# Performance work log

Hardware: AMD Instinct MI355X
Metric: run time of the kernel (lower is better)

## Reference

```python
import jax, jax.numpy as jnp
import numpy as np

N = 50000          # neuron_count
NNZ = 1_600_000    # edges (avg degree 32)
B = 32             # batch
L = 3              # CONNECTOME_LAYER_NUMBER


def setup_inputs() -> dict:
    key = jax.random.key(0)
    k1, k2, k3, k4, k5 = jax.random.split(key, 5)
    x = jax.random.normal(k1, (B, N), dtype=jnp.float32)
    adj_vals = jax.random.uniform(k2, (NNZ,), dtype=jnp.float32)
    w_vals = jax.random.uniform(k3, (NNZ,), dtype=jnp.float32)
    bias = jnp.ones((N,), dtype=jnp.float32)
    row = jax.random.randint(k4, (NNZ,), 0, N, dtype=jnp.int32)
    col = jax.random.randint(k5, (NNZ,), 0, N, dtype=jnp.int32)
    return {"x": x, "adj_vals": adj_vals, "w_vals": w_vals, "bias": bias,
            "row": row, "col": col}


def _spmm(vals, row, col, dense, n):
    # (sparse NxN) @ dense [N, B] via gather + segment_sum scatter
    contrib = vals[:, None] * dense[col]          # [nnz, B]
    return jax.ops.segment_sum(contrib, row, num_segments=n)


def reference(x, adj_vals, w_vals, bias, row, col):
    # Original per layer: x = ((A @ W) @ x^T)^T + bias.
    # We use associativity: (A @ W) @ x^T == A @ (W @ x^T), avoiding the
    # explicit SpGEMM while computing the same linear map.
    n = bias.shape[0]
    xt = x.T                                      # [N, B]
    for _ in range(L):
        wx = _spmm(w_vals, row, col, xt, n)       # W @ x^T -> [N, B]
        xt = _spmm(adj_vals, row, col, wx, n)     # A @ (W @ x^T)
        xt = xt + bias[:, None]                   # broadcast bias over batch
    return xt.T                                   # [B, N]
```

## Files before the change

kernel.cpp:

```cpp
#include <hip/hip_runtime.h>


#define NN 50000
#define NNZ_E 1600000
#define NB (NN * 32)
#define CHUNK 3072
#define NBLK1 ((NNZ_E + CHUNK - 1) / CHUNK)
#define NBIN ((NN + 127) / 128)
#define CAP2 5120
#define BCAP1 6144
#define LENE (NBIN * BCAP1)
#define BCAP 6144
#define LENP (NBIN * BCAP)
#define TIN_BLKS 196

__device__ __forceinline__ int clampi(int v, int hi) {
    v = v < 0 ? 0 : v;
    return v > hi ? hi : v;
}

__device__ __forceinline__ unsigned short f2h(float v) {
    union { _Float16 h; unsigned short u; } cv;
    cv.h = (_Float16)v;
    return cv.u;
}

__device__ __forceinline__ float kv_val(unsigned kv) {
    union { unsigned short u; _Float16 h; } cv;
    cv.u = (unsigned short)(kv >> 16);
    return (float)cv.h;
}

__global__ __launch_bounds__(256) void pass1_kernel(
        const int* __restrict__ row, const int* __restrict__ col,
        const float* __restrict__ a, const float* __restrict__ w,
        int* __restrict__ cursor, uint2* __restrict__ e1,
        const float* __restrict__ x, _Float16* __restrict__ xt) {
    __shared__ int h[NBIN];
    __shared__ int hscan[NBIN];
    __shared__ int hoff[NBIN];
    __shared__ int wsum[4];
    __shared__ unsigned sBuf[2 * CHUNK];
    int blk = blockIdx.x, tid = threadIdx.x;

    if (blk >= NBLK1) {
        _Float16* tl = (_Float16*)sBuf;
        int n0 = (blk - NBLK1) * 256;
        int n = n0 + tid;
#pragma unroll 8
        for (int b = 0; b < 32; ++b) {
            float v = (n < NN) ? x[b * NN + n] : 0.0f;
            tl[tid * 33 + b] = (_Float16)v;
        }
        __syncthreads();
#pragma unroll
        for (int k = 0; k < 4; ++k) {
            int o = (tid + 256 * k) * 8;
            int nl = o >> 5;
            int b0 = o & 31;
            int nn = n0 + nl;
            if (nn < NN) {
                union { uint4 u4; _Float16 hh[8]; } pk;
#pragma unroll
                for (int j = 0; j < 8; ++j) pk.hh[j] = tl[nl * 33 + b0 + j];
                *(uint4*)&xt[nn * 32 + b0] = pk.u4;
            }
        }
        return;
    }

    int base = blk * CHUNK;
    int n = NNZ_E - base; if (n > CHUNK) n = CHUNK;
    int nv = n >> 2;
    unsigned* sKey = sBuf;
    unsigned* sAW  = sBuf + CHUNK;

    for (int j = tid; j < NBIN; j += 256) h[j] = 0;
    __syncthreads();

    int rr[12], cc[12];
    unsigned aw2[12];
    int ne = 0;
    const int4*   rv4 = (const int4*)row;
    const int4*   cv4 = (const int4*)col;
    const float4* av4 = (const float4*)a;
    const float4* wv4 = (const float4*)w;
    int b4 = base >> 2;
    for (int t4 = tid; t4 < nv; t4 += 256) {
        int4 r = rv4[b4 + t4];
        int4 c = cv4[b4 + t4];
        float4 af = av4[b4 + t4];
        float4 wf = wv4[b4 + t4];
        rr[ne] = r.x; cc[ne] = c.x; aw2[ne] = ((unsigned)f2h(af.x) << 16) | f2h(wf.x); ++ne;
        rr[ne] = r.y; cc[ne] = c.y; aw2[ne] = ((unsigned)f2h(af.y) << 16) | f2h(wf.y); ++ne;
        rr[ne] = r.z; cc[ne] = c.z; aw2[ne] = ((unsigned)f2h(af.z) << 16) | f2h(wf.z); ++ne;
        rr[ne] = r.w; cc[ne] = c.w; aw2[ne] = ((unsigned)f2h(af.w) << 16) | f2h(wf.w); ++ne;
    }
    for (int i = 0; i < ne; ++i)
        atomicAdd(&h[clampi(rr[i], NN - 1) >> 7], 1);
    __syncthreads();

    int j0 = tid * 2, j1 = tid * 2 + 1;
    int c0 = (j0 < NBIN) ? h[j0] : 0;
    int c1 = (j1 < NBIN) ? h[j1] : 0;
    int tsum = c0 + c1;
    int lane = tid & 63, wid = tid >> 6;
    int inc = tsum;
#pragma unroll
    for (int off = 1; off < 64; off <<= 1) {
        int u = __shfl_up(inc, off, 64);
        if (lane >= off) inc += u;
    }
    if (lane == 63) wsum[wid] = inc;
    __syncthreads();
    int wo = 0;
#pragma unroll
    for (int q = 0; q < 4; ++q) if (q < wid) wo += wsum[q];
    int ex = wo + inc - tsum;

    if (j0 < NBIN) {
        hscan[j0] = ex;
        h[j0] = ex;
        int b0 = c0 ? atomicAdd(&cursor[j0], c0) : 0;
        hoff[j0] = j0 * BCAP1 + clampi(b0, BCAP1 - 1);
    }
    if (j1 < NBIN) {
        hscan[j1] = ex + c0;
        h[j1] = ex + c0;
        int b1 = c1 ? atomicAdd(&cursor[j1], c1) : 0;
        hoff[j1] = j1 * BCAP1 + clampi(b1, BCAP1 - 1);
    }
    __syncthreads();
    for (int i = 0; i < ne; ++i) {
        int r = clampi(rr[i], NN - 1);
        int c = clampi(cc[i], NN - 1);
        int bin = r >> 7;
        int p = atomicAdd(&h[bin], 1);
        p = clampi(p, n - 1);
        sKey[p] = ((unsigned)r << 16) | (unsigned)c;
        sAW[p] = aw2[i];
    }
    __syncthreads();
    for (int p = tid; p < n; p += 256) {
        unsigned key = sKey[p];
        int bin = (int)(key >> 23);
        int d = clampi(hoff[bin] + (p - hscan[bin]), LENE - 1);
        e1[d] = make_uint2(key, sAW[p]);
    }
}

__global__ __launch_bounds__(256) void pass2_kernel(
        const uint2* __restrict__ e1, const int* __restrict__ cursor,
        unsigned* __restrict__ kvA2, unsigned* __restrict__ kvW2,
        unsigned* __restrict__ row_desc) {
    __shared__ int rh[128];
    __shared__ int rs[128];
    __shared__ int cur[128];
    int bin = blockIdx.x, tid = threadIdx.x;
    int r0 = bin << 7;
    int rows = NN - r0; if (rows > 128) rows = 128;
    int ebase = bin * BCAP1;
    int size = clampi(cursor[bin], CAP2);
    int pbase = bin * BCAP;

    if (tid < 128) rh[tid] = 0;
    __syncthreads();
    for (int i = tid; i < size; i += 256)
        atomicAdd(&rh[(e1[ebase + i].x >> 16) & 127], 1);
    __syncthreads();
    int cnt  = (tid < 128) ? rh[tid] : 0;
    int plen = (cnt + 7) & ~7;
    if (tid < 128) rs[tid] = plen;
    __syncthreads();
    for (int off = 1; off < 128; off <<= 1) {
        int t = (tid >= off && tid < 128) ? rs[tid - off] : 0;
        __syncthreads();
        if (tid < 128) rs[tid] += t;
        __syncthreads();
    }
    int rofs = (tid < 128) ? clampi(rs[tid] - plen, BCAP - 8) : 0;
    if (tid < 128) cur[tid] = rofs;
    if (tid < rows)
        row_desc[r0 + tid] = (unsigned)(pbase + rofs) | ((unsigned)(plen >> 3) << 24);
    __syncthreads();
    for (int i = tid; i < size; i += 256) {
        uint2 e = e1[ebase + i];
        unsigned key = e.x;
        unsigned aw  = e.y;
        int rl = (key >> 16) & 127;
        int p = atomicAdd(&cur[rl], 1);
        p = clampi(p, BCAP - 1);
        unsigned c = key & 0xFFFFu;
        kvA2[pbase + p] = (aw & 0xFFFF0000u) | c;
        kvW2[pbase + p] = (aw << 16) | c;
    }
    __syncthreads();
    if (tid < rows) {
        int pl = (rh[tid] + 7) & ~7;
        for (int q = rh[tid]; q < pl; ++q) {
            int d = clampi(rofs + q, BCAP - 1);
            kvA2[pbase + d] = 0u;
            kvW2[pbase + d] = 0u;
        }
    }
}

template <int WITH_BIAS, int FINAL>
__global__ __launch_bounds__(256) void spmm_kernel(
        const uint2* __restrict__ kv2, const unsigned* __restrict__ row_desc,
        const unsigned* __restrict__ in32, unsigned* __restrict__ out32,
        const float* __restrict__ bias, float outScale, float biasScale,
        float* __restrict__ outf) {
    int t = blockIdx.x * 256 + threadIdx.x;
    int r = t >> 4;
    int l = t & 15;
    if (r >= NN) return;
    unsigned d = row_desc[r];
    int niter = (int)(d >> 24);
    int base2 = clampi((int)(d & 0xFFFFFFu), LENP - 8) >> 1;
    float accL = 0.0f, accH = 0.0f;
    uint2 k2[4];
    if (niter > 0) {
#pragma unroll
        for (int q = 0; q < 4; ++q) k2[q] = kv2[base2 + q];
    }
    for (int it = 0; it < niter; ++it) {
        unsigned k[8];
#pragma unroll
        for (int q = 0; q < 4; ++q) { k[2 * q] = k2[q].x; k[2 * q + 1] = k2[q].y; }
        unsigned gd[8];
#pragma unroll
        for (int j = 0; j < 8; ++j) gd[j] = in32[((k[j] & 0xFFFFu) << 4) + l];
        if (it + 1 < niter) {
            int nb2 = base2 + (it + 1) * 4;
#pragma unroll
            for (int q = 0; q < 4; ++q) k2[q] = kv2[nb2 + q];
        }
#pragma unroll
        for (int j = 0; j < 8; ++j) {
            float v = kv_val(k[j]);
            union { unsigned u; _Float16 h[2]; } cv;
            cv.u = gd[j];
            accL += v * (float)cv.h[0];
            accH += v * (float)cv.h[1];
        }
    }
    float rL = accL * outScale, rH = accH * outScale;
    if (WITH_BIAS) {
        float bb = bias[r] * biasScale;
        rL += bb; rH += bb;
    }
    if (FINAL) {
        outf[(2 * l) * NN + r]     = rL * 16777216.0f;
        outf[(2 * l + 1) * NN + r] = rH * 16777216.0f;
    } else {
        union { unsigned u; _Float16 h[2]; } o;
        o.h[0] = (_Float16)rL;
        o.h[1] = (_Float16)rH;
        out32[(r << 4) + l] = o.u;
    }
}

extern "C" void kernel_launch(void* const* d_in, const int* in_sizes, int n_in,
                              void* d_out, int out_size, void* d_ws, size_t ws_size,
                              hipStream_t stream) {
    const float* x        = (const float*)d_in[0];
    const float* adj_vals = (const float*)d_in[1];
    const float* w_vals   = (const float*)d_in[2];
    const float* bias     = (const float*)d_in[3];
    const int*   row      = (const int*)d_in[4];
    const int*   col      = (const int*)d_in[5];
    float* out = (float*)d_out;

    uint2*     e1        = (uint2*)d_ws;
    unsigned*  kvA2      = (unsigned*)(e1 + LENE);
    unsigned*  kvW2      = kvA2 + LENP;
    _Float16*  xt16      = (_Float16*)(kvW2 + LENP);
    _Float16*  tmp16     = xt16 + NB;
    int*       cursor    = (int*)(tmp16 + NB);
    unsigned*  row_desc  = (unsigned*)(cursor + NBIN + 8);

    const int BS = 256;
    const int grid_spmm = (NN * 16 + BS - 1) / BS;

    hipMemsetAsync(cursor, 0, NBIN * sizeof(int), stream);
    pass1_kernel<<<NBLK1 + TIN_BLKS, BS, 0, stream>>>(row, col, adj_vals, w_vals,
                                                      cursor, e1, x, xt16);
    pass2_kernel<<<NBIN, BS, 0, stream>>>(e1, cursor, kvA2, kvW2, row_desc);

    const uint2* kvA = (const uint2*)kvA2;
    const uint2* kvW = (const uint2*)kvW2;
    const unsigned* xt32  = (const unsigned*)xt16;
    unsigned*       xt32w = (unsigned*)xt16;
    const unsigned* tm32  = (const unsigned*)tmp16;
    unsigned*       tm32w = (unsigned*)tmp16;

    const float r256 = 1.0f / 256.0f;
    spmm_kernel<0, 0><<<grid_spmm, BS, 0, stream>>>(kvW, row_desc, xt32, tm32w,
                                                    nullptr, 1.0f, 0.0f, nullptr);
    spmm_kernel<1, 0><<<grid_spmm, BS, 0, stream>>>(kvA, row_desc, tm32, xt32w,
                                                    bias, r256, 1.0f / 256.0f, nullptr);
    spmm_kernel<0, 0><<<grid_spmm, BS, 0, stream>>>(kvW, row_desc, xt32, tm32w,
                                                    nullptr, 1.0f, 0.0f, nullptr);
    spmm_kernel<1, 0><<<grid_spmm, BS, 0, stream>>>(kvA, row_desc, tm32, xt32w,
                                                    bias, r256, 1.0f / 65536.0f, nullptr);
    spmm_kernel<0, 0><<<grid_spmm, BS, 0, stream>>>(kvW, row_desc, xt32, tm32w,
                                                    nullptr, 1.0f, 0.0f, nullptr);
    spmm_kernel<1, 1><<<grid_spmm, BS, 0, stream>>>(kvA, row_desc, tm32, xt32w,
                                                    bias, r256, 1.0f / 16777216.0f, out);
}
```

Baseline: 231.6 us.

## Scatter edges directly to global bins, dropping shared-memory staging and scan

Result: slower. 238.0 us (+2.7%).

```diff
diff --git a/kernel.cpp b/kernel.cpp
--- a/kernel.cpp
+++ b/kernel.cpp
@@ -36,11 +36,7 @@
         const float* __restrict__ a, const float* __restrict__ w,
         int* __restrict__ cursor, uint2* __restrict__ e1,
         const float* __restrict__ x, _Float16* __restrict__ xt) {
-    __shared__ int h[NBIN];
-    __shared__ int hscan[NBIN];
-    __shared__ int hoff[NBIN];
-    __shared__ int wsum[4];
-    __shared__ unsigned sBuf[2 * CHUNK];
+    __shared__ unsigned sBuf[256 * 33 / 2 + 8];
     int blk = blockIdx.x, tid = threadIdx.x;
 
     if (blk >= NBLK1) {
@@ -69,11 +65,10 @@
         return;
     }
 
+    int* h = (int*)sBuf;
     int base = blk * CHUNK;
     int n = NNZ_E - base; if (n > CHUNK) n = CHUNK;
     int nv = n >> 2;
-    unsigned* sKey = sBuf;
-    unsigned* sAW  = sBuf + CHUNK;
 
     for (int j = tid; j < NBIN; j += 256) h[j] = 0;
     __syncthreads();
@@ -101,51 +96,25 @@
     __syncthreads();
 
     int j0 = tid * 2, j1 = tid * 2 + 1;
-    int c0 = (j0 < NBIN) ? h[j0] : 0;
-    int c1 = (j1 < NBIN) ? h[j1] : 0;
-    int tsum = c0 + c1;
-    int lane = tid & 63, wid = tid >> 6;
-    int inc = tsum;
-#pragma unroll
-    for (int off = 1; off < 64; off <<= 1) {
-        int u = __shfl_up(inc, off, 64);
-        if (lane >= off) inc += u;
-    }
-    if (lane == 63) wsum[wid] = inc;
-    __syncthreads();
-    int wo = 0;
-#pragma unroll
-    for (int q = 0; q < 4; ++q) if (q < wid) wo += wsum[q];
-    int ex = wo + inc - tsum;
-
     if (j0 < NBIN) {
-        hscan[j0] = ex;
-        h[j0] = ex;
+        int c0 = h[j0];
         int b0 = c0 ? atomicAdd(&cursor[j0], c0) : 0;
-        hoff[j0] = j0 * BCAP1 + clampi(b0, BCAP1 - 1);
+        h[j0] = j0 * BCAP1 + clampi(b0, BCAP1 - 1);
     }
     if (j1 < NBIN) {
-        hscan[j1] = ex + c0;
-        h[j1] = ex + c0;
+        int c1 = h[j1];
         int b1 = c1 ? atomicAdd(&cursor[j1], c1) : 0;
-        hoff[j1] = j1 * BCAP1 + clampi(b1, BCAP1 - 1);
-    }
-    __syncthreads();
+        h[j1] = j1 * BCAP1 + clampi(b1, BCAP1 - 1);
+    }
+    __syncthreads();
+
     for (int i = 0; i < ne; ++i) {
         int r = clampi(rr[i], NN - 1);
         int c = clampi(cc[i], NN - 1);
         int bin = r >> 7;
-        int p = atomicAdd(&h[bin], 1);
-        p = clampi(p, n - 1);
-        sKey[p] = ((unsigned)r << 16) | (unsigned)c;
-        sAW[p] = aw2[i];
-    }
-    __syncthreads();
-    for (int p = tid; p < n; p += 256) {
-        unsigned key = sKey[p];
-        int bin = (int)(key >> 23);
-        int d = clampi(hoff[bin] + (p - hscan[bin]), LENE - 1);
-        e1[d] = make_uint2(key, sAW[p]);
+        int d = atomicAdd(&h[bin], 1);
+        d = clampi(d, LENE - 1);
+        e1[d] = make_uint2(((unsigned)r << 16) | (unsigned)c, aw2[i]);
     }
 }
 
```
